# Optimization experiments

Measured on AMD Instinct MI355X. Metric: run time of the kernel, lower is better.

## Reference

```python
import jax, jax.numpy as jnp
import numpy as np

D_MODEL = 1024
N_HEADS = 16
D_K = D_MODEL // N_HEADS  # 64
SCALE = 0.125             # attention_scale = 1/sqrt(d_k)
ROPE_BASE = 10000.0
NEG_INF = -1e30


def setup_inputs() -> dict:
    key = jax.random.key(0)
    k1, k2, k3 = jax.random.split(key, 3)
    B, S = 2, 2048
    x = jax.random.normal(k1, (B, S, D_MODEL), jnp.float32)
    # torch Linear(d_model, 3*d_model, bias=False): stored here as [in, out]
    w_qkv = jax.random.normal(k2, (D_MODEL, 3 * D_MODEL), jnp.float32) * (D_MODEL ** -0.5)
    w_o = jax.random.normal(k3, (D_MODEL, D_MODEL), jnp.float32) * (D_MODEL ** -0.5)
    return {"x": x, "w_qkv": w_qkv, "w_o": w_o}


def _rotary(x):
    # x: [B, H, S, D]; standard half-split rotary over sequence positions
    S, D = x.shape[2], x.shape[3]
    inv_freq = 1.0 / (ROPE_BASE ** (jnp.arange(0, D, 2, dtype=jnp.float32) / D))  # [D/2]
    freqs = jnp.arange(S, dtype=jnp.float32)[:, None] * inv_freq[None, :]          # [S, D/2]
    cos = jnp.cos(freqs)[None, None]  # [1,1,S,D/2]
    sin = jnp.sin(freqs)[None, None]
    x1, x2 = jnp.split(x, 2, axis=-1)
    return jnp.concatenate([x1 * cos + x2 * sin, -x1 * sin + x2 * cos], axis=-1).astype(x.dtype)


def reference(x, w_qkv, w_o):
    B, S, _ = x.shape
    qkv = x @ w_qkv                                        # [B,S,3*D_MODEL]
    qkv = qkv.reshape(B, S, 3, N_HEADS, D_K).transpose(2, 0, 3, 1, 4)  # [3,B,H,S,Dk]
    q, k, v = qkv[0], qkv[1], qkv[2]
    q = _rotary(q)
    k = _rotary(k)
    scores = jnp.einsum('bhqd,bhkd->bhqk', q, k) * SCALE   # [B,H,S,S]
    causal = jnp.tril(jnp.ones((S, S), dtype=bool))
    scores = jnp.where(causal, scores, NEG_INF)
    attn = jax.nn.softmax(scores, axis=-1)
    out = jnp.einsum('bhqk,bhkd->bhqd', attn, v)           # [B,H,S,Dk]
    out = out.transpose(0, 2, 1, 3).reshape(B, S, D_MODEL)
    return out @ w_o
```

## Files before the change

### kernel.cpp

```cpp
#include <hip/hip_runtime.h>

typedef short bf16x8 __attribute__((ext_vector_type(8)));
typedef short bf16x4 __attribute__((ext_vector_type(4)));
typedef float f32x4 __attribute__((ext_vector_type(4)));
typedef float f32x16 __attribute__((ext_vector_type(16)));
typedef int i32x4 __attribute__((ext_vector_type(4)));

#define DEVI static __device__ __forceinline__

DEVI unsigned short f2b(float f) {
  unsigned u = __float_as_uint(f);
  u += 0x7FFFu + ((u >> 16) & 1u);
  return (unsigned short)(u >> 16);
}

DEVI void gload16(const void* g, void* l) {
  __builtin_amdgcn_global_load_lds((const __attribute__((address_space(1))) void*)g,
                                   (__attribute__((address_space(3))) void*)l, 16, 0, 0);
}

DEVI void pl32swap(int a, int b, int& outa, int& outb) {
#if __has_builtin(__builtin_amdgcn_permlane32_swap)
  auto r = __builtin_amdgcn_permlane32_swap(a, b, false, false);
  outa = ((const int*)&r)[0];
  outb = ((const int*)&r)[1];
#else
  int bp = __shfl_xor(b, 32);
  int ap = __shfl_xor(a, 32);
  outa = (threadIdx.x & 32) ? bp : a;
  outb = (threadIdx.x & 32) ? b : ap;
#endif
}

DEVI float halfmax(float x) {
  int o0, o1;
  pl32swap(__float_as_int(x), __float_as_int(x), o0, o1);
  return fmaxf(__int_as_float(o0), __int_as_float(o1));
}
DEVI float halfsum(float x) {
  int o0, o1;
  pl32swap(__float_as_int(x), __float_as_int(x), o0, o1);
  return __int_as_float(o0) + __int_as_float(o1);
}

__global__ void rope_table_kernel(float2* __restrict__ cst) {
  int i = blockIdx.x * 256 + threadIdx.x;
  int s = i >> 5, j = i & 31;
  float inv = powf(10000.0f, -(float)j * (1.0f / 32.0f));
  float a = (float)s * inv;
  cst[i] = make_float2(cosf(a), sinf(a));
}

__global__ void cvt_x_kernel(const float* __restrict__ x, unsigned short* __restrict__ xb) {
  int i = blockIdx.x * 256 + threadIdx.x;
  float4 v = ((const float4*)x)[i];
  ushort4 o;
  o.x = f2b(v.x); o.y = f2b(v.y); o.z = f2b(v.z); o.w = f2b(v.w);
  ((ushort4*)xb)[i] = o;
}

__global__ void transpose_kernel(const float* __restrict__ W, unsigned short* __restrict__ WT,
                                 int K, int N) {
  __shared__ float tile[32][33];
  int n0 = blockIdx.x * 32, k0 = blockIdx.y * 32;
  int tx = threadIdx.x, ty = threadIdx.y;
#pragma unroll
  for (int i = 0; i < 32; i += 8)
    tile[ty + i][tx] = W[(size_t)(k0 + ty + i) * N + n0 + tx];
  __syncthreads();
#pragma unroll
  for (int i = 0; i < 32; i += 8)
    WT[(size_t)(n0 + ty + i) * K + k0 + tx] = f2b(tile[tx][ty + i]);
}

__global__ __launch_bounds__(512, 2) void gemm_qkv_kernel(
    const unsigned short* __restrict__ Xb, const unsigned short* __restrict__ WT,
    const float2* __restrict__ cst,
    unsigned short* __restrict__ Qb, unsigned short* __restrict__ Kb,
    unsigned short* __restrict__ VTb) {
  __shared__ unsigned short As[2][256 * 64];
  __shared__ unsigned short Bs[2][256 * 64];
  const int tid = threadIdx.x;
  const int lane = tid & 63, wid = tid >> 6;
  const int flat = blockIdx.y * 12 + blockIdx.x;
  const int nf = (flat & 7) * 24 + (flat >> 3);
  const int bx = nf % 12, by = nf / 12;
  const int m0 = by * 256, n0 = bx * 256;
  const int wr = wid >> 2, wc = wid & 3;
  const int srow = lane >> 3;
  const int scc = ((lane & 7) ^ srow) * 8;
  const int rx = lane & 7;

  f32x4 acc[8][4] = {};

  auto stageA = [&](int k0, int nb, int i) {
    const int c = i * 8 + wid;
    const int row = c * 8 + srow;
    gload16(Xb + (size_t)(m0 + row) * 1024 + k0 + scc, (char*)As[nb] + c * 1024);
  };
  auto stageB = [&](int k0, int nb, int i) {
    const int c = i * 8 + wid;
    const int row = c * 8 + srow;
    gload16(WT + (size_t)(n0 + row) * 1024 + k0 + scc, (char*)Bs[nb] + c * 1024);
  };
  auto loadA = [&](const unsigned short* Ab, int q, bf16x8 af[2][2]) {
#pragma unroll
    for (int kk = 0; kk < 2; ++kk) {
      const int cc = ((kk * 4 + (lane >> 4)) ^ rx) * 8;
#pragma unroll
      for (int miL = 0; miL < 2; ++miL)
        af[miL][kk] = *(const bf16x8*)&Ab[(wr * 128 + (q * 2 + miL) * 16 + (lane & 15)) * 64 + cc];
    }
  };

#define QKV_MFMA_QUAD(Q)                                                      \
  __builtin_amdgcn_s_barrier();                                               \
  asm volatile("s_waitcnt lgkmcnt(0)" ::: "memory");                          \
  __builtin_amdgcn_s_setprio(1);                                              \
  _Pragma("unroll") for (int kk = 0; kk < 2; ++kk)                            \
    _Pragma("unroll") for (int miL = 0; miL < 2; ++miL)                       \
      _Pragma("unroll") for (int ni = 0; ni < 4; ++ni)                        \
        acc[(Q) * 2 + miL][ni] = __builtin_amdgcn_mfma_f32_16x16x32_bf16(     \
            af[miL][kk], bf[ni][kk], acc[(Q) * 2 + miL][ni], 0, 0, 0);        \
  __builtin_amdgcn_s_setprio(0);                                              \
  __builtin_amdgcn_s_barrier();

#pragma unroll
  for (int i = 0; i < 4; ++i) stageB(0, 0, i);
#pragma unroll
  for (int i = 0; i < 4; ++i) stageA(0, 0, i);
#pragma unroll
  for (int i = 0; i < 4; ++i) stageB(64, 1, i);
  stageA(64, 1, 0); stageA(64, 1, 2);
  asm volatile("s_waitcnt vmcnt(6)" ::: "memory");
  __builtin_amdgcn_s_barrier();

  for (int t = 0; t < 16; ++t) {
    const int b = t & 1;
    const unsigned short* Ab = As[b];
    const unsigned short* Bb = Bs[b];
    const int k1 = (t + 1) * 64, k2 = (t + 2) * 64;
    bf16x8 bf[4][2], af[2][2];

#pragma unroll
    for (int kk = 0; kk < 2; ++kk) {
      const int cc = ((kk * 4 + (lane >> 4)) ^ rx) * 8;
#pragma unroll
      for (int ni = 0; ni < 4; ++ni)
        bf[ni][kk] = *(const bf16x8*)&Bb[(wc * 64 + ni * 16 + (lane & 15)) * 64 + cc];
    }
    loadA(Ab, 0, af);
    if (t + 1 < 16) { stageA(k1, b ^ 1, 1); stageA(k1, b ^ 1, 3); }
    QKV_MFMA_QUAD(0)

    loadA(Ab, 1, af);
    if (t + 2 < 16) { stageB(k2, b, 0); stageB(k2, b, 1); }
    QKV_MFMA_QUAD(1)

    loadA(Ab, 2, af);
    if (t + 2 < 16) { stageB(k2, b, 2); stageB(k2, b, 3); }
    QKV_MFMA_QUAD(2)

    loadA(Ab, 3, af);
    if (t + 2 < 16) { stageA(k2, b, 0); stageA(k2, b, 2); }
    __builtin_amdgcn_s_barrier();
    asm volatile("s_waitcnt lgkmcnt(0)" ::: "memory");
    __builtin_amdgcn_s_setprio(1);
#pragma unroll
    for (int kk = 0; kk < 2; ++kk)
#pragma unroll
      for (int miL = 0; miL < 2; ++miL)
#pragma unroll
        for (int ni = 0; ni < 4; ++ni)
          acc[6 + miL][ni] = __builtin_amdgcn_mfma_f32_16x16x32_bf16(
              af[miL][kk], bf[ni][kk], acc[6 + miL][ni], 0, 0, 0);
    __builtin_amdgcn_s_setprio(0);
    if (t + 2 < 16) asm volatile("s_waitcnt vmcnt(6)" ::: "memory");
    else            asm volatile("s_waitcnt vmcnt(0)" ::: "memory");
    __builtin_amdgcn_s_barrier();
  }
#undef QKV_MFMA_QUAD

  unsigned short* slab = (wid < 4) ? (&As[0][0] + wid * 8192)
                                   : (&Bs[0][0] + (wid - 4) * 8192);
  const int n_base = n0 + wc * 64;
  const int ty = n_base >> 10;
  const int h = (n_base & 1023) >> 6;
  const int qrow = (lane >> 4) << 2;
  const int l15 = lane & 15;
  const int rlane = lane >> 3, clane = lane & 7;

  if (ty < 2) {
    unsigned short* dst = (ty == 0) ? Qb : Kb;
#pragma unroll
    for (int g = 0; g < 2; ++g) {
      const int rowg = m0 + wr * 128 + g * 64;
      const int s_half = rowg & 2047, bb = rowg >> 11;
#pragma unroll
      for (int miL = 0; miL < 4; ++miL) {
        const int mi = g * 4 + miL;
        const int rl0 = miL * 16 + qrow;
#pragma unroll
        for (int r = 0; r < 4; ++r) {
#pragma unroll
          for (int ni = 0; ni < 2; ++ni) {
            const int j = ni * 16 + l15;
            const float2 cs = cst[(s_half + rl0 + r) * 32 + j];
            const float x1 = acc[mi][ni][r], x2 = acc[mi][ni + 2][r];
            slab[(rl0 + r) * 72 + j]      = f2b(x1 * cs.x + x2 * cs.y);
            slab[(rl0 + r) * 72 + j + 32] = f2b(-x1 * cs.y + x2 * cs.x);
          }
        }
      }
      unsigned short* dp = dst + ((size_t)(bb * 16 + h) * 2048 + s_half) * 64;
#pragma unroll
      for (int i = 0; i < 8; ++i) {
        const int row = i * 8 + rlane;
        const bf16x8 v = *(const bf16x8*)&slab[row * 72 + clane * 8];
        *(bf16x8*)&dp[row * 64 + clane * 8] = v;
      }
    }
  } else {
#pragma unroll
    for (int g = 0; g < 2; ++g) {
      const int rowg = m0 + wr * 128 + g * 64;
      const int s_half = rowg & 2047, bb = rowg >> 11;
#pragma unroll
      for (int miL = 0; miL < 4; ++miL) {
        const int mi = g * 4 + miL;
        const int rl0 = miL * 16 + qrow;
#pragma unroll
        for (int ni = 0; ni < 4; ++ni) {
          const int d = ni * 16 + l15;
#pragma unroll
          for (int r = 0; r < 4; ++r)
            slab[d * 72 + rl0 + r] = f2b(acc[mi][ni][r]);
        }
      }
      unsigned short* vp = VTb + (size_t)(bb * 16 + h) * 64 * 2048 + s_half;
#pragma unroll
      for (int i = 0; i < 8; ++i) {
        const int d = i * 8 + rlane;
        const bf16x8 v = *(const bf16x8*)&slab[d * 72 + clane * 8];
        *(bf16x8*)&vp[(size_t)d * 2048 + clane * 8] = v;
      }
    }
  }
}

DEVI void gemm_mainloop(const unsigned short* __restrict__ A, const unsigned short* __restrict__ B,
                        unsigned short* As, unsigned short* Bs,
                        int m0, int n0, int lane, int wid, int wr, int wc,
                        f32x4 acc[4][4]) {
  const int srow = lane >> 3;
  const int scc = ((lane & 7) ^ srow) * 8;
  const int rx = lane & 7;
  auto stage = [&](int k0, int nb) {
    unsigned short* Ad = As + nb * 8192;
    unsigned short* Bd = Bs + nb * 8192;
#pragma unroll
    for (int i = 0; i < 4; ++i) {
      const int c = i * 4 + wid;
      const int row = c * 8 + srow;
      gload16(A + (size_t)(m0 + row) * 1024 + k0 + scc, (char*)Ad + c * 1024);
      gload16(B + (size_t)(n0 + row) * 1024 + k0 + scc, (char*)Bd + c * 1024);
    }
  };
  auto compute = [&](int nb) {
    const unsigned short* Ab = As + nb * 8192;
    const unsigned short* Bb = Bs + nb * 8192;
#pragma unroll
    for (int kk = 0; kk < 64; kk += 32) {
      const int cc = (((kk >> 3) + (lane >> 4)) ^ rx) * 8;
      bf16x8 a[4], b[4];
#pragma unroll
      for (int mi = 0; mi < 4; ++mi)
        a[mi] = *(const bf16x8*)&Ab[(wr * 64 + mi * 16 + (lane & 15)) * 64 + cc];
#pragma unroll
      for (int ni = 0; ni < 4; ++ni)
        b[ni] = *(const bf16x8*)&Bb[(wc * 64 + ni * 16 + (lane & 15)) * 64 + cc];
      __builtin_amdgcn_s_setprio(1);
#pragma unroll
      for (int mi = 0; mi < 4; ++mi)
#pragma unroll
        for (int ni = 0; ni < 4; ++ni)
          acc[mi][ni] = __builtin_amdgcn_mfma_f32_16x16x32_bf16(a[mi], b[ni], acc[mi][ni], 0, 0, 0);
      __builtin_amdgcn_s_setprio(0);
    }
  };
  stage(0, 0);
  stage(64, 1);
  for (int t = 0; t < 15; ++t) {
    asm volatile("s_waitcnt vmcnt(8)" ::: "memory");
    __builtin_amdgcn_s_barrier();
    compute(t & 1);
    __builtin_amdgcn_s_barrier();
    if (t < 14) stage((t + 2) * 64, t & 1);
  }
  asm volatile("s_waitcnt vmcnt(0)" ::: "memory");
  __builtin_amdgcn_s_barrier();
  compute(1);
}

DEVI void stage128(const unsigned short* __restrict__ Kh, const unsigned short* __restrict__ Vh,
                   int kbase, unsigned char* buf, int tid) {
  const int r = tid >> 3, c = tid & 7, cc = c ^ (r & 7);
  const int dst = (tid & ~63) * 16;
#pragma unroll
  for (int q = 0; q < 2; ++q) {
    unsigned char* b = buf + q * 16384;
    gload16(Kh + (size_t)(kbase + q * 64 + r) * 64 + cc * 8, b + dst);
    gload16(Vh + (size_t)r * 2048 + kbase + q * 64 + cc * 8, b + 8192 + dst);
  }
}

DEVI void attn_sub(const unsigned char* __restrict__ bufK, const unsigned char* __restrict__ bufV,
                   const bf16x8 qf[4], int s32, int kglob, bool diag, int qg, int ln, int hi,
                   float& m2, float& l_run, f32x16& acc0, f32x16& acc1) {
  const float C = 0.125f * 1.44269504f;
  const int rx = ln & 7;
  bf16x8 kf[4];
#pragma unroll
  for (int j = 0; j < 4; ++j) {
    const int cc = (2 * j + hi) ^ rx;
    kf[j] = *(const bf16x8*)(bufK + (s32 * 32 + ln) * 128 + cc * 16);
  }
  bf16x8 v0[2], v1[2];
#pragma unroll
  for (int p = 0; p < 2; ++p) {
    const int cc = (4 * s32 + 2 * p + hi) ^ rx;
    v0[p] = *(const bf16x8*)(bufV + ln * 128 + cc * 16);
    v1[p] = *(const bf16x8*)(bufV + (ln + 32) * 128 + cc * 16);
  }

  f32x16 stv = {};
  __builtin_amdgcn_s_setprio(1);
  stv = __builtin_amdgcn_mfma_f32_32x32x16_bf16(kf[0], qf[0], stv, 0, 0, 0);
  stv = __builtin_amdgcn_mfma_f32_32x32x16_bf16(kf[1], qf[1], stv, 0, 0, 0);
  stv = __builtin_amdgcn_mfma_f32_32x32x16_bf16(kf[2], qf[2], stv, 0, 0, 0);
  stv = __builtin_amdgcn_mfma_f32_32x32x16_bf16(kf[3], qf[3], stv, 0, 0, 0);
  __builtin_amdgcn_s_setprio(0);

  float sraw[16];
#pragma unroll
  for (int r = 0; r < 16; ++r) sraw[r] = stv[r];
  if (diag) {
#pragma unroll
    for (int r = 0; r < 16; ++r) {
      const int kg = kglob + (r & 3) + ((r >> 2) << 3) + (hi << 2);
      if (kg > qg) sraw[r] = -1e30f;
    }
  }
  float mraw = sraw[0];
#pragma unroll
  for (int r = 1; r < 16; ++r) mraw = fmaxf(mraw, sraw[r]);
  const float mlc = mraw * C;
  if (__any(mlc > m2 + 11.5416f)) {
    const float mnew = fmaxf(m2, halfmax(mlc));
    const float sc = exp2f(m2 - mnew);
    l_run *= sc;
#pragma unroll
    for (int r = 0; r < 16; ++r) { acc0[r] *= sc; acc1[r] *= sc; }
    m2 = mnew;
  }
  float p[16], ps = 0.f;
#pragma unroll
  for (int r = 0; r < 16; ++r) { p[r] = exp2f(fmaf(sraw[r], C, -m2)); ps += p[r]; }
  l_run += ps;

  int cw[8];
#pragma unroll
  for (int i = 0; i < 8; ++i)
    asm("v_cvt_pk_bf16_f32 %0, %1, %2" : "=v"(cw[i]) : "v"(p[2 * i]), "v"(p[2 * i + 1]));
  int a0, a1, b0, b1, a2, a3, b2, b3;
  pl32swap(cw[0], cw[2], a0, b0);
  pl32swap(cw[1], cw[3], a1, b1);
  pl32swap(cw[4], cw[6], a2, b2);
  pl32swap(cw[5], cw[7], a3, b3);
  const bf16x8 pa0 = __builtin_bit_cast(bf16x8, (i32x4){a0, a1, b0, b1});
  const bf16x8 pa1 = __builtin_bit_cast(bf16x8, (i32x4){a2, a3, b2, b3});

  __builtin_amdgcn_s_setprio(1);
  acc0 = __builtin_amdgcn_mfma_f32_32x32x16_bf16(v0[0], pa0, acc0, 0, 0, 0);
  acc0 = __builtin_amdgcn_mfma_f32_32x32x16_bf16(v0[1], pa1, acc0, 0, 0, 0);
  acc1 = __builtin_amdgcn_mfma_f32_32x32x16_bf16(v1[0], pa0, acc1, 0, 0, 0);
  acc1 = __builtin_amdgcn_mfma_f32_32x32x16_bf16(v1[1], pa1, acc1, 0, 0, 0);
  __builtin_amdgcn_s_setprio(0);
}

DEVI void write_partial(float* M, int slot, const f32x16& a0, const f32x16& a1,
                        float m2, float l) {
#pragma unroll
  for (int r = 0; r < 16; ++r) { M[slot + r] = a0[r]; M[slot + 16 + r] = a1[r]; }
  M[slot + 32] = m2;
  M[slot + 33] = l;
}

DEVI void write_merged(unsigned short* __restrict__ Ob, const float* M, int slot,
                       const f32x16& acc0, const f32x16& acc1, float m2, float l_run,
                       int bh, int q0, int ln, int hi) {
  const float mp = M[slot + 32], lp = M[slot + 33];
  const float m = fmaxf(m2, mp);
  const float eo = exp2f(m2 - m), ep = exp2f(mp - m);
  const float il = 1.0f / (l_run * eo + lp * ep);
  const int b = bh >> 4, h = bh & 15;
  unsigned short* ob = Ob + ((size_t)(b * 2048 + q0 + ln)) * 1024 + h * 64;
#pragma unroll
  for (int g = 0; g < 4; ++g) {
    ushort4 o0, o1;
    o0.x = f2b((acc0[4 * g + 0] * eo + M[slot + 4 * g + 0] * ep) * il);
    o0.y = f2b((acc0[4 * g + 1] * eo + M[slot + 4 * g + 1] * ep) * il);
    o0.z = f2b((acc0[4 * g + 2] * eo + M[slot + 4 * g + 2] * ep) * il);
    o0.w = f2b((acc0[4 * g + 3] * eo + M[slot + 4 * g + 3] * ep) * il);
    o1.x = f2b((acc1[4 * g + 0] * eo + M[slot + 16 + 4 * g + 0] * ep) * il);
    o1.y = f2b((acc1[4 * g + 1] * eo + M[slot + 16 + 4 * g + 1] * ep) * il);
    o1.z = f2b((acc1[4 * g + 2] * eo + M[slot + 16 + 4 * g + 2] * ep) * il);
    o1.w = f2b((acc1[4 * g + 3] * eo + M[slot + 16 + 4 * g + 3] * ep) * il);
    *(ushort4*)&ob[8 * g + 4 * hi]      = o0;
    *(ushort4*)&ob[32 + 8 * g + 4 * hi] = o1;
  }
}

__global__ __launch_bounds__(512) void attn_kernel(
    const unsigned short* __restrict__ Qb, const unsigned short* __restrict__ Kb,
    const unsigned short* __restrict__ VTb, unsigned short* __restrict__ Ob) {
  __shared__ unsigned char smem[2][2][16384];
  const int tid = threadIdx.x;
  const int lane = tid & 63, wid = tid >> 6;
  const int ln = lane & 31, hi = lane >> 5;
  const int s = wid & 3, half = wid >> 2;
  const int bh = blockIdx.x;
  const int p = blockIdx.y;
  const int jA = 15 - p, jB = p;
  const unsigned short* Qh = Qb + (size_t)bh * 2048 * 64;
  const unsigned short* Kh = Kb + (size_t)bh * 2048 * 64;
  const unsigned short* Vh = VTb + (size_t)bh * 64 * 2048;

  f32x16 aA0 = {}, aA1 = {}, aB0 = {}, aB1 = {};
  float mA = -1e30f, lA = 0.f, mB = -1e30f, lB = 0.f;
  int it = 0;

  auto load_q = [&](int q0, bf16x8 qf[4]) {
    const unsigned short* pq = Qh + (size_t)(q0 + ln) * 64 + hi * 8;
#pragma unroll
    for (int t = 0; t < 4; ++t) qf[t] = *(const bf16x8*)(pq + t * 16);
  };
  auto run_phase = [&](int j, const bf16x8 qf[4], f32x16& acc0, f32x16& acc1,
                       float& m2, float& l_run, int q0, int nextFirst) {
    const int qg = q0 + ln;
    const int top = q0 >> 5;
    for (int kb = 0; kb <= j; ++kb, ++it) {
      const int nxt = (kb < j) ? (kb + 1) * 128 : nextFirst;
      if (nxt >= 0) stage128(Kh, Vh, nxt, &smem[(it + 1) & 1][0][0], tid);
      const unsigned char* bufK = &smem[it & 1][half][0];
      const unsigned char* bufV = bufK + 8192;
      const int t64 = 2 * kb + half;
#pragma unroll
      for (int s32 = 0; s32 < 2; ++s32) {
        const int g32 = 2 * t64 + s32;
        if (g32 <= top)
          attn_sub(bufK, bufV, qf, s32, g32 * 32, g32 == top, qg, ln, hi, m2, l_run, acc0, acc1);
      }
      __syncthreads();
    }
  };

  bf16x8 qfA[4];
  load_q(jA * 128 + s * 32, qfA);
  stage128(Kh, Vh, 0, &smem[0][0][0], tid);
  __syncthreads();
  run_phase(jA, qfA, aA0, aA1, mA, lA, jA * 128 + s * 32, 0);
  bf16x8 qfB[4];
  load_q(jB * 128 + s * 32, qfB);
  run_phase(jB, qfB, aB0, aB1, mB, lB, jB * 128 + s * 32, -1);

  lA = halfsum(lA);
  lB = halfsum(lB);

  float* M = (float*)&smem[0][0][0];
  const int slot = (s * 64 + lane) * 34;
  if (half == 1) write_partial(M, slot, aA0, aA1, mA, lA);
  __syncthreads();
  if (half == 0) write_merged(Ob, M, slot, aA0, aA1, mA, lA, bh, jA * 128 + s * 32, ln, hi);
  __syncthreads();
  if (half == 0) write_partial(M, slot, aB0, aB1, mB, lB);
  __syncthreads();
  if (half == 1) write_merged(Ob, M, slot, aB0, aB1, mB, lB, bh, jB * 128 + s * 32, ln, hi);
}

__global__ __launch_bounds__(256) void gemm_out_kernel(
    const unsigned short* __restrict__ Ob, const unsigned short* __restrict__ WoT,
    float* __restrict__ out) {
  __shared__ unsigned short As[2][128 * 64];
  __shared__ unsigned short Bs[2][128 * 64];
  const int lane = threadIdx.x & 63, wid = threadIdx.x >> 6;
  const int m0 = blockIdx.y * 128, n0 = blockIdx.x * 128;
  const int wr = wid >> 1, wc = wid & 1;
  f32x4 acc[4][4] = {};
  gemm_mainloop(Ob, WoT, &As[0][0], &Bs[0][0], m0, n0, lane, wid, wr, wc, acc);
#pragma unroll
  for (int mi = 0; mi < 4; ++mi) {
    const int mrow = m0 + wr * 64 + mi * 16 + ((lane >> 4) << 2);
#pragma unroll
    for (int ni = 0; ni < 4; ++ni) {
      const int n = n0 + wc * 64 + ni * 16 + (lane & 15);
#pragma unroll
      for (int r = 0; r < 4; ++r)
        out[(size_t)(mrow + r) * 1024 + n] = acc[mi][ni][r];
    }
  }
}

extern "C" void kernel_launch(void* const* d_in, const int* in_sizes, int n_in,
                              void* d_out, int out_size, void* d_ws, size_t ws_size,
                              hipStream_t stream) {
  const float* x     = (const float*)d_in[0];
  const float* w_qkv = (const float*)d_in[1];
  const float* w_o   = (const float*)d_in[2];
  float* out = (float*)d_out;
  char* ws = (char*)d_ws;

  const size_t MB = 1 << 20;
  float2* cst = (float2*)(ws);
  unsigned short* Xb  = (unsigned short*)(ws + (512 << 10));
  unsigned short* WqT = (unsigned short*)(ws + (512 << 10) + 8  * MB);
  unsigned short* WoT = (unsigned short*)(ws + (512 << 10) + 14 * MB);
  unsigned short* Qb  = (unsigned short*)(ws + (512 << 10) + 16 * MB);
  unsigned short* Kb  = (unsigned short*)(ws + (512 << 10) + 24 * MB);
  unsigned short* VTb = (unsigned short*)(ws + (512 << 10) + 32 * MB);
  unsigned short* Ob  = Xb;

  rope_table_kernel<<<dim3(256), dim3(256), 0, stream>>>(cst);
  cvt_x_kernel<<<dim3(4096), dim3(256), 0, stream>>>(x, Xb);
  transpose_kernel<<<dim3(96, 32), dim3(32, 8), 0, stream>>>(w_qkv, WqT, 1024, 3072);
  transpose_kernel<<<dim3(32, 32), dim3(32, 8), 0, stream>>>(w_o, WoT, 1024, 1024);
  gemm_qkv_kernel<<<dim3(12, 16), dim3(512), 0, stream>>>(Xb, WqT, cst, Qb, Kb, VTb);
  attn_kernel<<<dim3(32, 8), dim3(512), 0, stream>>>(Qb, Kb, VTb, Ob);
  gemm_out_kernel<<<dim3(8, 32), dim3(256), 0, stream>>>(Ob, WoT, out);
}
```

Before: 120.5 us.

## Retile QKV GEMM to 128x128, merge transposes, pair attention sub-tiles

The custom 256x256 QKV GEMM with its hand-scheduled pipeline is replaced by 128x128 tiles that reuse the shared gemm_mainloop, which gives 768 blocks instead of 192 for better CU fill. The two weight transpose launches are merged into one kernel. The attention inner loop now processes two 32-key sub-tiles together, interleaving their MFMAs and sharing one max/rescale step, and attn_kernel gets a 2-blocks-per-CU launch bound. Smaller GEMM tiles lower data reuse per block, and the paired attention path raises register pressure.

```diff
diff --git a/kernel.cpp b/kernel.cpp
--- a/kernel.cpp
+++ b/kernel.cpp
@@ -59,10 +59,15 @@
   ((ushort4*)xb)[i] = o;
 }
 
-__global__ void transpose_kernel(const float* __restrict__ W, unsigned short* __restrict__ WT,
-                                 int K, int N) {
+__global__ void transpose2_kernel(const float* __restrict__ W1, unsigned short* __restrict__ WT1,
+                                  const float* __restrict__ W2, unsigned short* __restrict__ WT2) {
   __shared__ float tile[32][33];
-  int n0 = blockIdx.x * 32, k0 = blockIdx.y * 32;
+  int bx = blockIdx.x;
+  const float* W; unsigned short* WT; int N;
+  if (bx < 96) { W = W1; WT = WT1; N = 3072; }
+  else         { W = W2; WT = WT2; N = 1024; bx -= 96; }
+  const int K = 1024;
+  int n0 = bx * 32, k0 = blockIdx.y * 32;
   int tx = threadIdx.x, ty = threadIdx.y;
 #pragma unroll
   for (int i = 0; i < 32; i += 8)
@@ -71,181 +76,6 @@
 #pragma unroll
   for (int i = 0; i < 32; i += 8)
     WT[(size_t)(n0 + ty + i) * K + k0 + tx] = f2b(tile[tx][ty + i]);
-}
-
-__global__ __launch_bounds__(512, 2) void gemm_qkv_kernel(
-    const unsigned short* __restrict__ Xb, const unsigned short* __restrict__ WT,
-    const float2* __restrict__ cst,
-    unsigned short* __restrict__ Qb, unsigned short* __restrict__ Kb,
-    unsigned short* __restrict__ VTb) {
-  __shared__ unsigned short As[2][256 * 64];
-  __shared__ unsigned short Bs[2][256 * 64];
-  const int tid = threadIdx.x;
-  const int lane = tid & 63, wid = tid >> 6;
-  const int flat = blockIdx.y * 12 + blockIdx.x;
-  const int nf = (flat & 7) * 24 + (flat >> 3);
-  const int bx = nf % 12, by = nf / 12;
-  const int m0 = by * 256, n0 = bx * 256;
-  const int wr = wid >> 2, wc = wid & 3;
-  const int srow = lane >> 3;
-  const int scc = ((lane & 7) ^ srow) * 8;
-  const int rx = lane & 7;
-
-  f32x4 acc[8][4] = {};
-
-  auto stageA = [&](int k0, int nb, int i) {
-    const int c = i * 8 + wid;
-    const int row = c * 8 + srow;
-    gload16(Xb + (size_t)(m0 + row) * 1024 + k0 + scc, (char*)As[nb] + c * 1024);
-  };
-  auto stageB = [&](int k0, int nb, int i) {
-    const int c = i * 8 + wid;
-    const int row = c * 8 + srow;
-    gload16(WT + (size_t)(n0 + row) * 1024 + k0 + scc, (char*)Bs[nb] + c * 1024);
-  };
-  auto loadA = [&](const unsigned short* Ab, int q, bf16x8 af[2][2]) {
-#pragma unroll
-    for (int kk = 0; kk < 2; ++kk) {
-      const int cc = ((kk * 4 + (lane >> 4)) ^ rx) * 8;
-#pragma unroll
-      for (int miL = 0; miL < 2; ++miL)
-        af[miL][kk] = *(const bf16x8*)&Ab[(wr * 128 + (q * 2 + miL) * 16 + (lane & 15)) * 64 + cc];
-    }
-  };
-
-#define QKV_MFMA_QUAD(Q)                                                      \
-  __builtin_amdgcn_s_barrier();                                               \
-  asm volatile("s_waitcnt lgkmcnt(0)" ::: "memory");                          \
-  __builtin_amdgcn_s_setprio(1);                                              \
-  _Pragma("unroll") for (int kk = 0; kk < 2; ++kk)                            \
-    _Pragma("unroll") for (int miL = 0; miL < 2; ++miL)                       \
-      _Pragma("unroll") for (int ni = 0; ni < 4; ++ni)                        \
-        acc[(Q) * 2 + miL][ni] = __builtin_amdgcn_mfma_f32_16x16x32_bf16(     \
-            af[miL][kk], bf[ni][kk], acc[(Q) * 2 + miL][ni], 0, 0, 0);        \
-  __builtin_amdgcn_s_setprio(0);                                              \
-  __builtin_amdgcn_s_barrier();
-
-#pragma unroll
-  for (int i = 0; i < 4; ++i) stageB(0, 0, i);
-#pragma unroll
-  for (int i = 0; i < 4; ++i) stageA(0, 0, i);
-#pragma unroll
-  for (int i = 0; i < 4; ++i) stageB(64, 1, i);
-  stageA(64, 1, 0); stageA(64, 1, 2);
-  asm volatile("s_waitcnt vmcnt(6)" ::: "memory");
-  __builtin_amdgcn_s_barrier();
-
-  for (int t = 0; t < 16; ++t) {
-    const int b = t & 1;
-    const unsigned short* Ab = As[b];
-    const unsigned short* Bb = Bs[b];
-    const int k1 = (t + 1) * 64, k2 = (t + 2) * 64;
-    bf16x8 bf[4][2], af[2][2];
-
-#pragma unroll
-    for (int kk = 0; kk < 2; ++kk) {
-      const int cc = ((kk * 4 + (lane >> 4)) ^ rx) * 8;
-#pragma unroll
-      for (int ni = 0; ni < 4; ++ni)
-        bf[ni][kk] = *(const bf16x8*)&Bb[(wc * 64 + ni * 16 + (lane & 15)) * 64 + cc];
-    }
-    loadA(Ab, 0, af);
-    if (t + 1 < 16) { stageA(k1, b ^ 1, 1); stageA(k1, b ^ 1, 3); }
-    QKV_MFMA_QUAD(0)
-
-    loadA(Ab, 1, af);
-    if (t + 2 < 16) { stageB(k2, b, 0); stageB(k2, b, 1); }
-    QKV_MFMA_QUAD(1)
-
-    loadA(Ab, 2, af);
-    if (t + 2 < 16) { stageB(k2, b, 2); stageB(k2, b, 3); }
-    QKV_MFMA_QUAD(2)
-
-    loadA(Ab, 3, af);
-    if (t + 2 < 16) { stageA(k2, b, 0); stageA(k2, b, 2); }
-    __builtin_amdgcn_s_barrier();
-    asm volatile("s_waitcnt lgkmcnt(0)" ::: "memory");
-    __builtin_amdgcn_s_setprio(1);
-#pragma unroll
-    for (int kk = 0; kk < 2; ++kk)
-#pragma unroll
-      for (int miL = 0; miL < 2; ++miL)
-#pragma unroll
-        for (int ni = 0; ni < 4; ++ni)
-          acc[6 + miL][ni] = __builtin_amdgcn_mfma_f32_16x16x32_bf16(
-              af[miL][kk], bf[ni][kk], acc[6 + miL][ni], 0, 0, 0);
-    __builtin_amdgcn_s_setprio(0);
-    if (t + 2 < 16) asm volatile("s_waitcnt vmcnt(6)" ::: "memory");
-    else            asm volatile("s_waitcnt vmcnt(0)" ::: "memory");
-    __builtin_amdgcn_s_barrier();
-  }
-#undef QKV_MFMA_QUAD
-
-  unsigned short* slab = (wid < 4) ? (&As[0][0] + wid * 8192)
-                                   : (&Bs[0][0] + (wid - 4) * 8192);
-  const int n_base = n0 + wc * 64;
-  const int ty = n_base >> 10;
-  const int h = (n_base & 1023) >> 6;
-  const int qrow = (lane >> 4) << 2;
-  const int l15 = lane & 15;
-  const int rlane = lane >> 3, clane = lane & 7;
-
-  if (ty < 2) {
-    unsigned short* dst = (ty == 0) ? Qb : Kb;
-#pragma unroll
-    for (int g = 0; g < 2; ++g) {
-      const int rowg = m0 + wr * 128 + g * 64;
-      const int s_half = rowg & 2047, bb = rowg >> 11;
-#pragma unroll
-      for (int miL = 0; miL < 4; ++miL) {
-        const int mi = g * 4 + miL;
-        const int rl0 = miL * 16 + qrow;
-#pragma unroll
-        for (int r = 0; r < 4; ++r) {
-#pragma unroll
-          for (int ni = 0; ni < 2; ++ni) {
-            const int j = ni * 16 + l15;
-            const float2 cs = cst[(s_half + rl0 + r) * 32 + j];
-            const float x1 = acc[mi][ni][r], x2 = acc[mi][ni + 2][r];
-            slab[(rl0 + r) * 72 + j]      = f2b(x1 * cs.x + x2 * cs.y);
-            slab[(rl0 + r) * 72 + j + 32] = f2b(-x1 * cs.y + x2 * cs.x);
-          }
-        }
-      }
-      unsigned short* dp = dst + ((size_t)(bb * 16 + h) * 2048 + s_half) * 64;
-#pragma unroll
-      for (int i = 0; i < 8; ++i) {
-        const int row = i * 8 + rlane;
-        const bf16x8 v = *(const bf16x8*)&slab[row * 72 + clane * 8];
-        *(bf16x8*)&dp[row * 64 + clane * 8] = v;
-      }
-    }
-  } else {
-#pragma unroll
-    for (int g = 0; g < 2; ++g) {
-      const int rowg = m0 + wr * 128 + g * 64;
-      const int s_half = rowg & 2047, bb = rowg >> 11;
-#pragma unroll
-      for (int miL = 0; miL < 4; ++miL) {
-        const int mi = g * 4 + miL;
-        const int rl0 = miL * 16 + qrow;
-#pragma unroll
-        for (int ni = 0; ni < 4; ++ni) {
-          const int d = ni * 16 + l15;
-#pragma unroll
-          for (int r = 0; r < 4; ++r)
-            slab[d * 72 + rl0 + r] = f2b(acc[mi][ni][r]);
-        }
-      }
-      unsigned short* vp = VTb + (size_t)(bb * 16 + h) * 64 * 2048 + s_half;
-#pragma unroll
-      for (int i = 0; i < 8; ++i) {
-        const int d = i * 8 + rlane;
-        const bf16x8 v = *(const bf16x8*)&slab[d * 72 + clane * 8];
-        *(bf16x8*)&vp[(size_t)d * 2048 + clane * 8] = v;
-      }
-    }
-  }
 }
 
 DEVI void gemm_mainloop(const unsigned short* __restrict__ A, const unsigned short* __restrict__ B,
@@ -302,6 +132,79 @@
   compute(1);
 }
 
+__global__ __launch_bounds__(256, 2) void gemm_qkv_kernel(
+    const unsigned short* __restrict__ Xb, const unsigned short* __restrict__ WT,
+    const float2* __restrict__ cst,
+    unsigned short* __restrict__ Qb, unsigned short* __restrict__ Kb,
+    unsigned short* __restrict__ VTb) {
+  __shared__ unsigned short As[2][8192];
+  __shared__ unsigned short Bs[2][8192];
+  const int lane = threadIdx.x & 63, wid = threadIdx.x >> 6;
+  const int flat = blockIdx.y * 24 + blockIdx.x;
+  const int nf = (flat & 7) * 96 + (flat >> 3);
+  const int bx = nf % 24, by = nf / 24;
+  const int m0 = by * 128, n0 = bx * 128;
+  const int wr = wid >> 1, wc = wid & 1;
+  f32x4 acc[4][4] = {};
+  gemm_mainloop(Xb, WT, &As[0][0], &Bs[0][0], m0, n0, lane, wid, wr, wc, acc);
+
+  __syncthreads();
+  unsigned short* slab = (unsigned short*)((char*)&As[0][0] + wid * 9216);
+  const int n_base = n0 + wc * 64;
+  const int ty = n_base >> 10;
+  const int h = (n_base & 1023) >> 6;
+  const int qrow = (lane >> 4) << 2;
+  const int l15 = lane & 15;
+  const int rlane = lane >> 3, clane = lane & 7;
+  const int rowg = m0 + wr * 64;
+  const int s_half = rowg & 2047, bb = rowg >> 11;
+
+  if (ty < 2) {
+    unsigned short* dst = (ty == 0) ? Qb : Kb;
+#pragma unroll
+    for (int mi = 0; mi < 4; ++mi) {
+      const int rl0 = mi * 16 + qrow;
+#pragma unroll
+      for (int r = 0; r < 4; ++r) {
+#pragma unroll
+        for (int ni = 0; ni < 2; ++ni) {
+          const int j = ni * 16 + l15;
+          const float2 cs = cst[(s_half + rl0 + r) * 32 + j];
+          const float x1 = acc[mi][ni][r], x2 = acc[mi][ni + 2][r];
+          slab[(rl0 + r) * 72 + j]      = f2b(x1 * cs.x + x2 * cs.y);
+          slab[(rl0 + r) * 72 + j + 32] = f2b(-x1 * cs.y + x2 * cs.x);
+        }
+      }
+    }
+    unsigned short* dp = dst + ((size_t)(bb * 16 + h) * 2048 + s_half) * 64;
+#pragma unroll
+    for (int i = 0; i < 8; ++i) {
+      const int row = i * 8 + rlane;
+      const bf16x8 v = *(const bf16x8*)&slab[row * 72 + clane * 8];
+      *(bf16x8*)&dp[row * 64 + clane * 8] = v;
+    }
+  } else {
+#pragma unroll
+    for (int mi = 0; mi < 4; ++mi) {
+      const int rl0 = mi * 16 + qrow;
+#pragma unroll
+      for (int ni = 0; ni < 4; ++ni) {
+        const int d = ni * 16 + l15;
+#pragma unroll
+        for (int r = 0; r < 4; ++r)
+          slab[d * 72 + rl0 + r] = f2b(acc[mi][ni][r]);
+      }
+    }
+    unsigned short* vp = VTb + (size_t)(bb * 16 + h) * 64 * 2048 + s_half;
+#pragma unroll
+    for (int i = 0; i < 8; ++i) {
+      const int d = i * 8 + rlane;
+      const bf16x8 v = *(const bf16x8*)&slab[d * 72 + clane * 8];
+      *(bf16x8*)&vp[(size_t)d * 2048 + clane * 8] = v;
+    }
+  }
+}
+
 DEVI void stage128(const unsigned short* __restrict__ Kh, const unsigned short* __restrict__ Vh,
                    int kbase, unsigned char* buf, int tid) {
   const int r = tid >> 3, c = tid & 7, cc = c ^ (r & 7);
@@ -314,46 +217,62 @@
   }
 }
 
-DEVI void attn_sub(const unsigned char* __restrict__ bufK, const unsigned char* __restrict__ bufV,
-                   const bf16x8 qf[4], int s32, int kglob, bool diag, int qg, int ln, int hi,
-                   float& m2, float& l_run, f32x16& acc0, f32x16& acc1) {
+DEVI void build_pa(const f32x16& s, bf16x8& pa0, bf16x8& pa1) {
+  int cw[8];
+#pragma unroll
+  for (int i = 0; i < 8; ++i)
+    asm("v_cvt_pk_bf16_f32 %0, %1, %2" : "=v"(cw[i]) : "v"(s[2 * i]), "v"(s[2 * i + 1]));
+  int a0, a1, b0, b1, a2, a3, b2, b3;
+  pl32swap(cw[0], cw[2], a0, b0);
+  pl32swap(cw[1], cw[3], a1, b1);
+  pl32swap(cw[4], cw[6], a2, b2);
+  pl32swap(cw[5], cw[7], a3, b3);
+  pa0 = __builtin_bit_cast(bf16x8, (i32x4){a0, a1, b0, b1});
+  pa1 = __builtin_bit_cast(bf16x8, (i32x4){a2, a3, b2, b3});
+}
+
+DEVI void attn_pair(const unsigned char* __restrict__ bufK, const unsigned char* __restrict__ bufV,
+                    const bf16x8 qf[4], int kglob, bool diag1, int qg, int ln, int hi,
+                    float& m2, float& l_run, f32x16& acc0, f32x16& acc1) {
   const float C = 0.125f * 1.44269504f;
   const int rx = ln & 7;
-  bf16x8 kf[4];
-#pragma unroll
-  for (int j = 0; j < 4; ++j) {
-    const int cc = (2 * j + hi) ^ rx;
-    kf[j] = *(const bf16x8*)(bufK + (s32 * 32 + ln) * 128 + cc * 16);
-  }
-  bf16x8 v0[2], v1[2];
-#pragma unroll
-  for (int p = 0; p < 2; ++p) {
-    const int cc = (4 * s32 + 2 * p + hi) ^ rx;
-    v0[p] = *(const bf16x8*)(bufV + ln * 128 + cc * 16);
-    v1[p] = *(const bf16x8*)(bufV + (ln + 32) * 128 + cc * 16);
-  }
-
-  f32x16 stv = {};
-  __builtin_amdgcn_s_setprio(1);
-  stv = __builtin_amdgcn_mfma_f32_32x32x16_bf16(kf[0], qf[0], stv, 0, 0, 0);
-  stv = __builtin_amdgcn_mfma_f32_32x32x16_bf16(kf[1], qf[1], stv, 0, 0, 0);
-  stv = __builtin_amdgcn_mfma_f32_32x32x16_bf16(kf[2], qf[2], stv, 0, 0, 0);
-  stv = __builtin_amdgcn_mfma_f32_32x32x16_bf16(kf[3], qf[3], stv, 0, 0, 0);
-  __builtin_amdgcn_s_setprio(0);
-
-  float sraw[16];
-#pragma unroll
-  for (int r = 0; r < 16; ++r) sraw[r] = stv[r];
-  if (diag) {
+  f32x16 s0 = {}, s1 = {};
+  {
+    bf16x8 k0[4], k1[4];
+#pragma unroll
+    for (int j = 0; j < 4; ++j) {
+      const int cc = (2 * j + hi) ^ rx;
+      k0[j] = *(const bf16x8*)(bufK + ln * 128 + cc * 16);
+      k1[j] = *(const bf16x8*)(bufK + (32 + ln) * 128 + cc * 16);
+    }
+    __builtin_amdgcn_s_setprio(1);
+#pragma unroll
+    for (int j = 0; j < 4; ++j) {
+      s0 = __builtin_amdgcn_mfma_f32_32x32x16_bf16(k0[j], qf[j], s0, 0, 0, 0);
+      s1 = __builtin_amdgcn_mfma_f32_32x32x16_bf16(k1[j], qf[j], s1, 0, 0, 0);
+    }
+    __builtin_amdgcn_s_setprio(0);
+  }
+  bf16x8 va[2][2], vb[2][2];
+#pragma unroll
+  for (int st = 0; st < 2; ++st)
+#pragma unroll
+    for (int p = 0; p < 2; ++p) {
+      const int cc = (4 * st + 2 * p + hi) ^ rx;
+      va[st][p] = *(const bf16x8*)(bufV + ln * 128 + cc * 16);
+      vb[st][p] = *(const bf16x8*)(bufV + (ln + 32) * 128 + cc * 16);
+    }
+
+  if (diag1) {
 #pragma unroll
     for (int r = 0; r < 16; ++r) {
-      const int kg = kglob + (r & 3) + ((r >> 2) << 3) + (hi << 2);
-      if (kg > qg) sraw[r] = -1e30f;
-    }
-  }
-  float mraw = sraw[0];
-#pragma unroll
-  for (int r = 1; r < 16; ++r) mraw = fmaxf(mraw, sraw[r]);
+      const int kg = kglob + 32 + (r & 3) + ((r >> 2) << 3) + (hi << 2);
+      if (kg > qg) s1[r] = -1e30f;
+    }
+  }
+  float mraw = fmaxf(s0[0], s1[0]);
+#pragma unroll
+  for (int r = 1; r < 16; ++r) mraw = fmaxf(mraw, fmaxf(s0[r], s1[r]));
   const float mlc = mraw * C;
   if (__any(mlc > m2 + 11.5416f)) {
     const float mnew = fmaxf(m2, halfmax(mlc));
@@ -363,28 +282,83 @@
     for (int r = 0; r < 16; ++r) { acc0[r] *= sc; acc1[r] *= sc; }
     m2 = mnew;
   }
-  float p[16], ps = 0.f;
-#pragma unroll
-  for (int r = 0; r < 16; ++r) { p[r] = exp2f(fmaf(sraw[r], C, -m2)); ps += p[r]; }
+  float ps0 = 0.f, ps1 = 0.f;
+#pragma unroll
+  for (int r = 0; r < 16; ++r) { s0[r] = exp2f(fmaf(s0[r], C, -m2)); ps0 += s0[r]; }
+#pragma unroll
+  for (int r = 0; r < 16; ++r) { s1[r] = exp2f(fmaf(s1[r], C, -m2)); ps1 += s1[r]; }
+  l_run += ps0 + ps1;
+
+  bf16x8 pa[2][2];
+  build_pa(s0, pa[0][0], pa[0][1]);
+  build_pa(s1, pa[1][0], pa[1][1]);
+
+  __builtin_amdgcn_s_setprio(1);
+#pragma unroll
+  for (int st = 0; st < 2; ++st) {
+    acc0 = __builtin_amdgcn_mfma_f32_32x32x16_bf16(va[st][0], pa[st][0], acc0, 0, 0, 0);
+    acc1 = __builtin_amdgcn_mfma_f32_32x32x16_bf16(vb[st][0], pa[st][0], acc1, 0, 0, 0);
+    acc0 = __builtin_amdgcn_mfma_f32_32x32x16_bf16(va[st][1], pa[st][1], acc0, 0, 0, 0);
+    acc1 = __builtin_amdgcn_mfma_f32_32x32x16_bf16(vb[st][1], pa[st][1], acc1, 0, 0, 0);
+  }
+  __builtin_amdgcn_s_setprio(0);
+}
+
+DEVI void attn_single(const unsigned char* __restrict__ bufK, const unsigned char* __restrict__ bufV,
+                      const bf16x8 qf[4], int kglob, int qg, int ln, int hi,
+                      float& m2, float& l_run, f32x16& acc0, f32x16& acc1) {
+  const float C = 0.125f * 1.44269504f;
+  const int rx = ln & 7;
+  f32x16 s0 = {};
+  {
+    bf16x8 k0[4];
+#pragma unroll
+    for (int j = 0; j < 4; ++j) {
+      const int cc = (2 * j + hi) ^ rx;
+      k0[j] = *(const bf16x8*)(bufK + ln * 128 + cc * 16);
+    }
+    __builtin_amdgcn_s_setprio(1);
+#pragma unroll
+    for (int j = 0; j < 4; ++j)
+      s0 = __builtin_amdgcn_mfma_f32_32x32x16_bf16(k0[j], qf[j], s0, 0, 0, 0);
+    __builtin_amdgcn_s_setprio(0);
+  }
+  bf16x8 va[2], vb[2];
+#pragma unroll
+  for (int p = 0; p < 2; ++p) {
+    const int cc = (2 * p + hi) ^ rx;
+    va[p] = *(const bf16x8*)(bufV + ln * 128 + cc * 16);
+    vb[p] = *(const bf16x8*)(bufV + (ln + 32) * 128 + cc * 16);
+  }
+#pragma unroll
+  for (int r = 0; r < 16; ++r) {
+    const int kg = kglob + (r & 3) + ((r >> 2) << 3) + (hi << 2);
+    if (kg > qg) s0[r] = -1e30f;
+  }
+  float mraw = s0[0];
+#pragma unroll
+  for (int r = 1; r < 16; ++r) mraw = fmaxf(mraw, s0[r]);
+  const float mlc = mraw * C;
+  if (__any(mlc > m2 + 11.5416f)) {
+    const float mnew = fmaxf(m2, halfmax(mlc));
+    const float sc = exp2f(m2 - mnew);
+    l_run *= sc;
+#pragma unroll
+    for (int r = 0; r < 16; ++r) { acc0[r] *= sc; acc1[r] *= sc; }
+    m2 = mnew;
+  }
+  float ps = 0.f;
+#pragma unroll
+  for (int r = 0; r < 16; ++r) { s0[r] = exp2f(fmaf(s0[r], C, -m2)); ps += s0[r]; }
   l_run += ps;
 
-  int cw[8];
-#pragma unroll
-  for (int i = 0; i < 8; ++i)
-    asm("v_cvt_pk_bf16_f32 %0, %1, %2" : "=v"(cw[i]) : "v"(p[2 * i]), "v"(p[2 * i + 1]));
-  int a0, a1, b0, b1, a2, a3, b2, b3;
-  pl32swap(cw[0], cw[2], a0, b0);
-  pl32swap(cw[1], cw[3], a1, b1);
-  pl32swap(cw[4], cw[6], a2, b2);
-  pl32swap(cw[5], cw[7], a3, b3);
-  const bf16x8 pa0 = __builtin_bit_cast(bf16x8, (i32x4){a0, a1, b0, b1});
-  const bf16x8 pa1 = __builtin_bit_cast(bf16x8, (i32x4){a2, a3, b2, b3});
-
+  bf16x8 pa0, pa1;
+  build_pa(s0, pa0, pa1);
   __builtin_amdgcn_s_setprio(1);
-  acc0 = __builtin_amdgcn_mfma_f32_32x32x16_bf16(v0[0], pa0, acc0, 0, 0, 0);
-  acc0 = __builtin_amdgcn_mfma_f32_32x32x16_bf16(v0[1], pa1, acc0, 0, 0, 0);
-  acc1 = __builtin_amdgcn_mfma_f32_32x32x16_bf16(v1[0], pa0, acc1, 0, 0, 0);
-  acc1 = __builtin_amdgcn_mfma_f32_32x32x16_bf16(v1[1], pa1, acc1, 0, 0, 0);
+  acc0 = __builtin_amdgcn_mfma_f32_32x32x16_bf16(va[0], pa0, acc0, 0, 0, 0);
+  acc1 = __builtin_amdgcn_mfma_f32_32x32x16_bf16(vb[0], pa0, acc1, 0, 0, 0);
+  acc0 = __builtin_amdgcn_mfma_f32_32x32x16_bf16(va[1], pa1, acc0, 0, 0, 0);
+  acc1 = __builtin_amdgcn_mfma_f32_32x32x16_bf16(vb[1], pa1, acc1, 0, 0, 0);
   __builtin_amdgcn_s_setprio(0);
 }
 
@@ -421,7 +395,7 @@
   }
 }
 
-__global__ __launch_bounds__(512) void attn_kernel(
+__global__ __launch_bounds__(512, 2) void attn_kernel(
     const unsigned short* __restrict__ Qb, const unsigned short* __restrict__ Kb,
     const unsigned short* __restrict__ VTb, unsigned short* __restrict__ Ob) {
   __shared__ unsigned char smem[2][2][16384];
@@ -455,12 +429,12 @@
       const unsigned char* bufK = &smem[it & 1][half][0];
       const unsigned char* bufV = bufK + 8192;
       const int t64 = 2 * kb + half;
-#pragma unroll
-      for (int s32 = 0; s32 < 2; ++s32) {
-        const int g32 = 2 * t64 + s32;
-        if (g32 <= top)
-          attn_sub(bufK, bufV, qf, s32, g32 * 32, g32 == top, qg, ln, hi, m2, l_run, acc0, acc1);
-      }
+      const int nv = top - 2 * t64 + 1;
+      if (nv >= 2)
+        attn_pair(bufK, bufV, qf, t64 * 64, top == 2 * t64 + 1, qg, ln, hi,
+                  m2, l_run, acc0, acc1);
+      else if (nv == 1)
+        attn_single(bufK, bufV, qf, t64 * 64, qg, ln, hi, m2, l_run, acc0, acc1);
       __syncthreads();
     }
   };
@@ -491,8 +465,8 @@
 __global__ __launch_bounds__(256) void gemm_out_kernel(
     const unsigned short* __restrict__ Ob, const unsigned short* __restrict__ WoT,
     float* __restrict__ out) {
-  __shared__ unsigned short As[2][128 * 64];
-  __shared__ unsigned short Bs[2][128 * 64];
+  __shared__ unsigned short As[2][8192];
+  __shared__ unsigned short Bs[2][8192];
   const int lane = threadIdx.x & 63, wid = threadIdx.x >> 6;
   const int m0 = blockIdx.y * 128, n0 = blockIdx.x * 128;
   const int wr = wid >> 1, wc = wid & 1;
@@ -532,9 +506,8 @@
 
   rope_table_kernel<<<dim3(256), dim3(256), 0, stream>>>(cst);
   cvt_x_kernel<<<dim3(4096), dim3(256), 0, stream>>>(x, Xb);
-  transpose_kernel<<<dim3(96, 32), dim3(32, 8), 0, stream>>>(w_qkv, WqT, 1024, 3072);
-  transpose_kernel<<<dim3(32, 32), dim3(32, 8), 0, stream>>>(w_o, WoT, 1024, 1024);
-  gemm_qkv_kernel<<<dim3(12, 16), dim3(512), 0, stream>>>(Xb, WqT, cst, Qb, Kb, VTb);
+  transpose2_kernel<<<dim3(128, 32), dim3(32, 8), 0, stream>>>(w_qkv, WqT, w_o, WoT);
+  gemm_qkv_kernel<<<dim3(24, 32), dim3(256), 0, stream>>>(Xb, WqT, cst, Qb, Kb, VTb);
   attn_kernel<<<dim3(32, 8), dim3(512), 0, stream>>>(Qb, Kb, VTb, Ob);
   gemm_out_kernel<<<dim3(8, 32), dim3(256), 0, stream>>>(Ob, WoT, out);
 }
```

Measured after the change: 119.3 us. Within noise of the previous version (-0.9%).
